# Kernel optimization log

Hardware: AMD Instinct MI355X
Metric: run time of the kernel (lower is better)

The kernel has to match this reference:

```python
import jax, jax.numpy as jnp
import numpy as np

N_NODES = 40000
N_EDGES = 640000
IN_DIM, H_DIM, OUT_DIM = 128, 128, 64


def setup_inputs() -> dict:
    key = jax.random.key(0)
    ks = jax.random.split(key, 16)
    x = jax.random.normal(ks[0], (N_NODES, IN_DIM), dtype=jnp.float32)
    edge_index = jax.random.randint(ks[1], (2, N_EDGES), 0, N_NODES, dtype=jnp.int64)
    dims = [(IN_DIM, H_DIM), (H_DIM, H_DIM), (H_DIM, OUT_DIM)]
    inp = {"x": x, "edge_index": edge_index}
    for l, (di, do) in enumerate(dims):
        s = 1.0 / np.sqrt(di)
        inp[f"Wr{l}"] = jax.random.uniform(ks[2 + 3 * l], (di, do), jnp.float32, -s, s)  # lin_rel weight
        inp[f"br{l}"] = jax.random.uniform(ks[3 + 3 * l], (do,), jnp.float32, -s, s)     # lin_rel bias
        inp[f"Ws{l}"] = jax.random.uniform(ks[4 + 3 * l], (di, do), jnp.float32, -s, s)  # lin_root weight (no bias)
    return inp


def _graph_conv(x, src, dst, Wr, br, Ws):
    # PyG GraphConv (aggr='add'): out = lin_rel(sum_{j in N(i)} x_j) + lin_root(x_i)
    agg = jax.ops.segment_sum(x[src], dst, num_segments=N_NODES)  # [N, d_in]
    return agg @ Wr + br + x @ Ws


def reference(x, edge_index, Wr0, br0, Ws0, Wr1, br1, Ws1, Wr2, br2, Ws2):
    src, dst = edge_index[0], edge_index[1]
    h = x
    for Wr, br, Ws in ((Wr0, br0, Ws0), (Wr1, br1, Ws1), (Wr2, br2, Ws2)):
        h = _graph_conv(h, src, dst, Wr, br, Ws)
        h = jax.nn.relu(h)
        # dropout p=0 / eval mode -> identity
    return jax.nn.log_softmax(h, axis=1)
```

## Files before the change

kernel.cpp:

```cpp
#include <hip/hip_runtime.h>
#include <hip/hip_bf16.h>


#define N_NODES 40000
#define N_EDGES 640000
#define PAD_NODES 40064
#define DEG_CAP   40960
#define ROW_CAP   64

typedef float v4f __attribute__((ext_vector_type(4)));
typedef short short8 __attribute__((ext_vector_type(8)));

__device__ inline unsigned short f2b(float f) {
    unsigned u = __float_as_uint(f);
    return (unsigned short)((u + 0x7fffu + ((u >> 16) & 1u)) >> 16);
}

__global__ __launch_bounds__(256) void prep_kernel(const float* __restrict__ Wr0, const float* __restrict__ Ws0,
                                                   const float* __restrict__ Wr1, const float* __restrict__ Ws1,
                                                   const float* __restrict__ Wr2, const float* __restrict__ Ws2,
                                                   unsigned short* __restrict__ Wt0,
                                                   unsigned short* __restrict__ Wt1,
                                                   unsigned short* __restrict__ Wt2,
                                                   int* __restrict__ deg) {
    int tid = blockIdx.x * 256 + threadIdx.x;
    if (tid < DEG_CAP / 4) {
        ((int4*)deg)[tid] = make_int4(0, 0, 0, 0);
    } else {
        int t = tid - DEG_CAP / 4;
        if (t < 32768) {
            int n = t >> 7, k = t & 127;
            const float* W = (n < 128) ? Wr0 : Ws0;
            Wt0[t] = f2b(W[k * 128 + (n & 127)]);
        } else if (t < 65536) {
            int u = t - 32768;
            int n = u >> 7, k = u & 127;
            const float* W = (n < 128) ? Wr1 : Ws1;
            Wt1[u] = f2b(W[k * 128 + (n & 127)]);
        } else if (t < 81920) {
            int u = t - 65536;
            int n = u >> 7, k = u & 127;
            const float* W = (n < 64) ? Wr2 : Ws2;
            Wt2[u] = f2b(W[k * 64 + (n & 63)]);
        }
    }
}

__global__ __launch_bounds__(256) void place_kernel(const int* __restrict__ src,
                                                    const int* __restrict__ dst,
                                                    int* __restrict__ deg,
                                                    int* __restrict__ esrc) {
    int e = blockIdx.x * 256 + threadIdx.x;
    if (e < N_EDGES) {
        int d = dst[e];
        int r = atomicAdd(&deg[d], 1);
        if (r < ROW_CAP) esrc[(size_t)d * ROW_CAP + r] = src[e];
    }
}

template <int DO, bool F32>
__global__ __launch_bounds__(256) void mm_kernel(const void* __restrict__ Ain,
                                                 const unsigned short* __restrict__ Wt,
                                                 unsigned short* __restrict__ T,
                                                 unsigned short* __restrict__ S) {
    __shared__ unsigned short As[128 * 128];
    __shared__ unsigned short Bs[128 * 128];

    const int tid = threadIdx.x;
    const int m0  = blockIdx.x * 128;
    const int n0  = blockIdx.y * 128;

    if (F32) {
        const float4* Xg = (const float4*)Ain;
#pragma unroll
        for (int i = 0; i < 16; i++) {
            int idx = i * 256 + tid;
            int row = idx >> 5, c4 = idx & 31;
            int gr = m0 + row;
            if (gr > N_NODES - 1) gr = N_NODES - 1;
            float4 v = Xg[(size_t)gr * 32 + c4];
            uint2 p;
            p.x = (unsigned)f2b(v.x) | ((unsigned)f2b(v.y) << 16);
            p.y = (unsigned)f2b(v.z) | ((unsigned)f2b(v.w) << 16);
            ((uint2*)As)[idx] = p;
        }
    } else {
        const uint4* ga = (const uint4*)((const unsigned short*)Ain + (size_t)m0 * 128);
#pragma unroll
        for (int i = 0; i < 8; i++) ((uint4*)As)[i * 256 + tid] = ga[i * 256 + tid];
    }
    {
        const uint4* gb = (const uint4*)(Wt + (size_t)n0 * 128);
#pragma unroll
        for (int i = 0; i < 8; i++) ((uint4*)Bs)[i * 256 + tid] = gb[i * 256 + tid];
    }
    __syncthreads();

    const int wave = tid >> 6;
    const int lane = tid & 63;
    const int wr   = (wave >> 1) * 64;
    const int wc   = (wave & 1) * 64;
    const int qm   = lane & 15;
    const int k8   = (lane >> 4) * 8;

    v4f acc[4][4];
#pragma unroll
    for (int i = 0; i < 4; i++)
#pragma unroll
        for (int j = 0; j < 4; j++) acc[i][j] = (v4f)(0.0f);

#pragma unroll
    for (int ks = 0; ks < 4; ks++) {
        short8 af[4], bf[4];
#pragma unroll
        for (int i = 0; i < 4; i++) {
            af[i] = *(const short8*)(const void*)(As + (wr + i * 16 + qm) * 128 + ks * 32 + k8);
            bf[i] = *(const short8*)(const void*)(Bs + (wc + i * 16 + qm) * 128 + ks * 32 + k8);
        }
#pragma unroll
        for (int mi = 0; mi < 4; mi++)
#pragma unroll
            for (int ni = 0; ni < 4; ni++)
                acc[mi][ni] = __builtin_amdgcn_mfma_f32_16x16x32_bf16(af[mi], bf[ni], acc[mi][ni], 0, 0, 0);
    }

#pragma unroll
    for (int mi = 0; mi < 4; mi++) {
        const int nodeBase = m0 + wr + mi * 16 + ((lane >> 4) << 2);
#pragma unroll
        for (int r = 0; r < 4; r++) {
            const int node = nodeBase + r;
            if (node <= N_NODES) {
                const bool real = (node < N_NODES);
#pragma unroll
                for (int ni = 0; ni < 4; ni++) {
                    const int c = wc + ni * 16 + qm;
                    const unsigned short hv = real ? f2b(acc[mi][ni][r]) : (unsigned short)0;
                    if (DO == 128) {
                        (blockIdx.y ? S : T)[(size_t)node * 128 + c] = hv;
                    } else {
                        if (c < 64) T[(size_t)node * 64 + c] = hv;
                        else        S[(size_t)node * 64 + (c - 64)] = hv;
                    }
                }
            }
        }
    }
}

__device__ inline void addp(float* a, uint4 q) {
    a[0] += __uint_as_float(q.x << 16); a[1] += __uint_as_float(q.x & 0xffff0000u);
    a[2] += __uint_as_float(q.y << 16); a[3] += __uint_as_float(q.y & 0xffff0000u);
    a[4] += __uint_as_float(q.z << 16); a[5] += __uint_as_float(q.z & 0xffff0000u);
    a[6] += __uint_as_float(q.w << 16); a[7] += __uint_as_float(q.w & 0xffff0000u);
}

template <int DO, bool LAST>
__global__ __launch_bounds__(256) void aggregate_kernel(const unsigned short* __restrict__ T,
                                                        const unsigned short* __restrict__ S,
                                                        const float* __restrict__ br,
                                                        const int* __restrict__ deg,
                                                        const int* __restrict__ esrc,
                                                        unsigned short* __restrict__ Hout,
                                                        float* __restrict__ Fout) {
    constexpr int TPN = DO / 8;
    constexpr int G   = 256 / TPN;
    const int lane = threadIdx.x % TPN;
    const int n    = blockIdx.x * G + threadIdx.x / TPN;

    int cnt = deg[n];
    if (cnt > ROW_CAP) cnt = ROW_CAP;
    const int* erow = esrc + (size_t)n * ROW_CAP;
    const uint4* T4 = (const uint4*)T;

    const uint4  sv = ((const uint4*)S)[(size_t)n * TPN + lane];
    const float4 b0 = ((const float4*)br)[lane * 2];
    const float4 b1 = ((const float4*)br)[lane * 2 + 1];

    float acc[8] = {0.f, 0.f, 0.f, 0.f, 0.f, 0.f, 0.f, 0.f};
    for (int o = 0; o < cnt; o += 8) {
        int4 i0 = *(const int4*)(erow + o);
        int4 i1 = *(const int4*)(erow + o + 4);
        i0.x = (o + 0 < cnt) ? i0.x : N_NODES;
        i0.y = (o + 1 < cnt) ? i0.y : N_NODES;
        i0.z = (o + 2 < cnt) ? i0.z : N_NODES;
        i0.w = (o + 3 < cnt) ? i0.w : N_NODES;
        i1.x = (o + 4 < cnt) ? i1.x : N_NODES;
        i1.y = (o + 5 < cnt) ? i1.y : N_NODES;
        i1.z = (o + 6 < cnt) ? i1.z : N_NODES;
        i1.w = (o + 7 < cnt) ? i1.w : N_NODES;
        uint4 q0 = T4[(size_t)i0.x * TPN + lane];
        uint4 q1 = T4[(size_t)i0.y * TPN + lane];
        uint4 q2 = T4[(size_t)i0.z * TPN + lane];
        uint4 q3 = T4[(size_t)i0.w * TPN + lane];
        uint4 q4 = T4[(size_t)i1.x * TPN + lane];
        uint4 q5 = T4[(size_t)i1.y * TPN + lane];
        uint4 q6 = T4[(size_t)i1.z * TPN + lane];
        uint4 q7 = T4[(size_t)i1.w * TPN + lane];
        addp(acc, q0); addp(acc, q1); addp(acc, q2); addp(acc, q3);
        addp(acc, q4); addp(acc, q5); addp(acc, q6); addp(acc, q7);
    }
    addp(acc, sv);

    float v[8];
    v[0] = fmaxf(acc[0] + b0.x, 0.f); v[1] = fmaxf(acc[1] + b0.y, 0.f);
    v[2] = fmaxf(acc[2] + b0.z, 0.f); v[3] = fmaxf(acc[3] + b0.w, 0.f);
    v[4] = fmaxf(acc[4] + b1.x, 0.f); v[5] = fmaxf(acc[5] + b1.y, 0.f);
    v[6] = fmaxf(acc[6] + b1.z, 0.f); v[7] = fmaxf(acc[7] + b1.w, 0.f);

    if (LAST) {
        float m = v[0];
#pragma unroll
        for (int i = 1; i < 8; i++) m = fmaxf(m, v[i]);
#pragma unroll
        for (int off = 4; off; off >>= 1) m = fmaxf(m, __shfl_xor(m, off, 64));
        float es = 0.f;
#pragma unroll
        for (int i = 0; i < 8; i++) es += expf(v[i] - m);
#pragma unroll
        for (int off = 4; off; off >>= 1) es += __shfl_xor(es, off, 64);
        float lse = m + logf(es);
        float4 o0 = make_float4(v[0] - lse, v[1] - lse, v[2] - lse, v[3] - lse);
        float4 o1 = make_float4(v[4] - lse, v[5] - lse, v[6] - lse, v[7] - lse);
        ((float4*)Fout)[(size_t)n * 16 + lane * 2]     = o0;
        ((float4*)Fout)[(size_t)n * 16 + lane * 2 + 1] = o1;
    } else {
        uint4 o;
        o.x = (unsigned)f2b(v[0]) | ((unsigned)f2b(v[1]) << 16);
        o.y = (unsigned)f2b(v[2]) | ((unsigned)f2b(v[3]) << 16);
        o.z = (unsigned)f2b(v[4]) | ((unsigned)f2b(v[5]) << 16);
        o.w = (unsigned)f2b(v[6]) | ((unsigned)f2b(v[7]) << 16);
        ((uint4*)Hout)[(size_t)n * TPN + lane] = o;
    }
}


extern "C" void kernel_launch(void* const* d_in, const int* in_sizes, int n_in,
                              void* d_out, int out_size, void* d_ws, size_t ws_size,
                              hipStream_t stream) {
    const float* x    = (const float*)d_in[0];
    const int*   eidx = (const int*)d_in[1];
    const float* Wr0  = (const float*)d_in[2];
    const float* br0  = (const float*)d_in[3];
    const float* Ws0  = (const float*)d_in[4];
    const float* Wr1  = (const float*)d_in[5];
    const float* br1  = (const float*)d_in[6];
    const float* Ws1  = (const float*)d_in[7];
    const float* Wr2  = (const float*)d_in[8];
    const float* br2  = (const float*)d_in[9];
    const float* Ws2  = (const float*)d_in[10];
    float* out = (float*)d_out;

    const int* src = eidx;
    const int* dst = eidx + N_EDGES;

    auto align = [](size_t v) { return (v + 255) & ~(size_t)255; };
    char* w = (char*)d_ws;
    int* deg  = (int*)w;  w += align(sizeof(int) * DEG_CAP);
    int* esrc = (int*)w;  w += align(sizeof(int) * (size_t)N_NODES * ROW_CAP);
    unsigned short* H1b = (unsigned short*)w;  w += align(2ull * PAD_NODES * 128);
    unsigned short* H2b = (unsigned short*)w;  w += align(2ull * PAD_NODES * 128);
    unsigned short* Wt0 = (unsigned short*)w;  w += align(2ull * 256 * 128);
    unsigned short* Wt1 = (unsigned short*)w;  w += align(2ull * 256 * 128);
    unsigned short* Wt2 = (unsigned short*)w;  w += align(2ull * 128 * 128);
    unsigned short* T   = (unsigned short*)w;  w += align(2ull * PAD_NODES * 128);
    unsigned short* Sb  = (unsigned short*)w;  w += align(2ull * PAD_NODES * 128);
    (void)ws_size; (void)n_in; (void)in_sizes; (void)out_size;

    prep_kernel<<<(DEG_CAP / 4 + 81920 + 255) / 256, 256, 0, stream>>>(
        Wr0, Ws0, Wr1, Ws1, Wr2, Ws2, Wt0, Wt1, Wt2, deg);

    place_kernel<<<(N_EDGES + 255) / 256, 256, 0, stream>>>(src, dst, deg, esrc);

    mm_kernel<128, true><<<dim3(PAD_NODES / 128, 2), 256, 0, stream>>>(x, Wt0, T, Sb);
    aggregate_kernel<128, false><<<N_NODES / 16, 256, 0, stream>>>(T, Sb, br0, deg, esrc, H1b, nullptr);

    mm_kernel<128, false><<<dim3(PAD_NODES / 128, 2), 256, 0, stream>>>(H1b, Wt1, T, Sb);
    aggregate_kernel<128, false><<<N_NODES / 16, 256, 0, stream>>>(T, Sb, br1, deg, esrc, H2b, nullptr);

    mm_kernel<64, false><<<dim3(PAD_NODES / 128, 1), 256, 0, stream>>>(H2b, Wt2, T, Sb);
    aggregate_kernel<64, true><<<N_NODES / 32, 256, 0, stream>>>(T, Sb, br2, deg, esrc, nullptr, out);
}
```

Before: 215.2 us.

## Pad edge rows once, vectorize edge placement, use packed float2 accumulation

Edge placement now handles four edges per thread with int4 loads. A new pad kernel fills the tail of each node's neighbor row up to a multiple of 8 with the dummy node index, so the three aggregate kernels no longer do per-element bounds selects. Accumulators become float2 vectors so the compiler can emit packed FP32 adds. The cost is one extra small kernel launch plus extra scattered writes. Placement also assumes the edge count divides evenly by 1024.

Result: slower. 222.6 us (+3.5%).

```diff
diff --git a/kernel.cpp b/kernel.cpp
--- a/kernel.cpp
+++ b/kernel.cpp
@@ -9,6 +9,7 @@
 #define ROW_CAP   64
 
 typedef float v4f __attribute__((ext_vector_type(4)));
+typedef float v2f __attribute__((ext_vector_type(2)));
 typedef short short8 __attribute__((ext_vector_type(8)));
 
 __device__ inline unsigned short f2b(float f) {
@@ -50,11 +51,23 @@
                                                     const int* __restrict__ dst,
                                                     int* __restrict__ deg,
                                                     int* __restrict__ esrc) {
-    int e = blockIdx.x * 256 + threadIdx.x;
-    if (e < N_EDGES) {
-        int d = dst[e];
-        int r = atomicAdd(&deg[d], 1);
-        if (r < ROW_CAP) esrc[(size_t)d * ROW_CAP + r] = src[e];
+    int e4 = blockIdx.x * 256 + threadIdx.x;
+    int4 s = ((const int4*)src)[e4];
+    int4 d = ((const int4*)dst)[e4];
+    int r;
+    r = atomicAdd(&deg[d.x], 1); if (r < ROW_CAP) esrc[(size_t)d.x * ROW_CAP + r] = s.x;
+    r = atomicAdd(&deg[d.y], 1); if (r < ROW_CAP) esrc[(size_t)d.y * ROW_CAP + r] = s.y;
+    r = atomicAdd(&deg[d.z], 1); if (r < ROW_CAP) esrc[(size_t)d.z * ROW_CAP + r] = s.z;
+    r = atomicAdd(&deg[d.w], 1); if (r < ROW_CAP) esrc[(size_t)d.w * ROW_CAP + r] = s.w;
+}
+
+__global__ __launch_bounds__(256) void pad_kernel(const int* __restrict__ deg,
+                                                  int* __restrict__ esrc) {
+    int n = blockIdx.x * 256 + threadIdx.x;
+    if (n < N_NODES) {
+        int c = deg[n]; if (c > ROW_CAP) c = ROW_CAP;
+        int pc = (c + 7) & ~7;
+        for (int r = c; r < pc; r++) esrc[(size_t)n * ROW_CAP + r] = N_NODES;
     }
 }
 
@@ -148,11 +161,12 @@
     }
 }
 
-__device__ inline void addp(float* a, uint4 q) {
-    a[0] += __uint_as_float(q.x << 16); a[1] += __uint_as_float(q.x & 0xffff0000u);
-    a[2] += __uint_as_float(q.y << 16); a[3] += __uint_as_float(q.y & 0xffff0000u);
-    a[4] += __uint_as_float(q.z << 16); a[5] += __uint_as_float(q.z & 0xffff0000u);
-    a[6] += __uint_as_float(q.w << 16); a[7] += __uint_as_float(q.w & 0xffff0000u);
+__device__ inline void addp(v2f* a, uint4 q) {
+    v2f t0 = { __uint_as_float(q.x << 16), __uint_as_float(q.x & 0xffff0000u) };
+    v2f t1 = { __uint_as_float(q.y << 16), __uint_as_float(q.y & 0xffff0000u) };
+    v2f t2 = { __uint_as_float(q.z << 16), __uint_as_float(q.z & 0xffff0000u) };
+    v2f t3 = { __uint_as_float(q.w << 16), __uint_as_float(q.w & 0xffff0000u) };
+    a[0] += t0; a[1] += t1; a[2] += t2; a[3] += t3;
 }
 
 template <int DO, bool LAST>
@@ -170,6 +184,7 @@
 
     int cnt = deg[n];
     if (cnt > ROW_CAP) cnt = ROW_CAP;
+    const int pcnt = (cnt + 7) & ~7;
     const int* erow = esrc + (size_t)n * ROW_CAP;
     const uint4* T4 = (const uint4*)T;
 
@@ -177,18 +192,13 @@
     const float4 b0 = ((const float4*)br)[lane * 2];
     const float4 b1 = ((const float4*)br)[lane * 2 + 1];
 
-    float acc[8] = {0.f, 0.f, 0.f, 0.f, 0.f, 0.f, 0.f, 0.f};
-    for (int o = 0; o < cnt; o += 8) {
+    v2f acc[4];
+    acc[0] = (v2f)(0.0f); acc[1] = (v2f)(0.0f);
+    acc[2] = (v2f)(0.0f); acc[3] = (v2f)(0.0f);
+
+    for (int o = 0; o < pcnt; o += 8) {
         int4 i0 = *(const int4*)(erow + o);
         int4 i1 = *(const int4*)(erow + o + 4);
-        i0.x = (o + 0 < cnt) ? i0.x : N_NODES;
-        i0.y = (o + 1 < cnt) ? i0.y : N_NODES;
-        i0.z = (o + 2 < cnt) ? i0.z : N_NODES;
-        i0.w = (o + 3 < cnt) ? i0.w : N_NODES;
-        i1.x = (o + 4 < cnt) ? i1.x : N_NODES;
-        i1.y = (o + 5 < cnt) ? i1.y : N_NODES;
-        i1.z = (o + 6 < cnt) ? i1.z : N_NODES;
-        i1.w = (o + 7 < cnt) ? i1.w : N_NODES;
         uint4 q0 = T4[(size_t)i0.x * TPN + lane];
         uint4 q1 = T4[(size_t)i0.y * TPN + lane];
         uint4 q2 = T4[(size_t)i0.z * TPN + lane];
@@ -203,10 +213,10 @@
     addp(acc, sv);
 
     float v[8];
-    v[0] = fmaxf(acc[0] + b0.x, 0.f); v[1] = fmaxf(acc[1] + b0.y, 0.f);
-    v[2] = fmaxf(acc[2] + b0.z, 0.f); v[3] = fmaxf(acc[3] + b0.w, 0.f);
-    v[4] = fmaxf(acc[4] + b1.x, 0.f); v[5] = fmaxf(acc[5] + b1.y, 0.f);
-    v[6] = fmaxf(acc[6] + b1.z, 0.f); v[7] = fmaxf(acc[7] + b1.w, 0.f);
+    v[0] = fmaxf(acc[0].x + b0.x, 0.f); v[1] = fmaxf(acc[0].y + b0.y, 0.f);
+    v[2] = fmaxf(acc[1].x + b0.z, 0.f); v[3] = fmaxf(acc[1].y + b0.w, 0.f);
+    v[4] = fmaxf(acc[2].x + b1.x, 0.f); v[5] = fmaxf(acc[2].y + b1.y, 0.f);
+    v[6] = fmaxf(acc[3].x + b1.z, 0.f); v[7] = fmaxf(acc[3].y + b1.w, 0.f);
 
     if (LAST) {
         float m = v[0];
@@ -270,7 +280,8 @@
     prep_kernel<<<(DEG_CAP / 4 + 81920 + 255) / 256, 256, 0, stream>>>(
         Wr0, Ws0, Wr1, Ws1, Wr2, Ws2, Wt0, Wt1, Wt2, deg);
 
-    place_kernel<<<(N_EDGES + 255) / 256, 256, 0, stream>>>(src, dst, deg, esrc);
+    place_kernel<<<N_EDGES / 4 / 256, 256, 0, stream>>>(src, dst, deg, esrc);
+    pad_kernel<<<(N_NODES + 255) / 256, 256, 0, stream>>>(deg, esrc);
 
     mm_kernel<128, true><<<dim3(PAD_NODES / 128, 2), 256, 0, stream>>>(x, Wt0, T, Sb);
     aggregate_kernel<128, false><<<N_NODES / 16, 256, 0, stream>>>(T, Sb, br0, deg, esrc, H1b, nullptr);
```
